# Kernel optimization log

Hardware: AMD Instinct MI355X
Metric: run time of the kernel (lower is better)

Reference implementation:

```python
import jax, jax.numpy as jnp
import numpy as np
from jax import lax

D_STATE = 16
D_CONV = 4
EXPAND = 2


def setup_inputs() -> dict:
    key = jax.random.key(0)
    ks = jax.random.split(key, 12)
    B, C, H, W = 8, 192, 32, 32
    d_inner = EXPAND * C            # 384
    dt_rank = (C + 15) // 16        # 12
    s = lambda k, shape, sc=0.02: jax.random.normal(k, shape, jnp.float32) * sc
    return {
        "x": jax.random.normal(ks[0], (B, C, H, W), jnp.float32),
        # proj_in: 1x1 Conv2d (in_ch -> out_ch)
        "proj_w": s(ks[1], (C, C)),
        "proj_b": s(ks[2], (C,)),
        # Mamba params (mamba_ssm defaults, biases per reference impl)
        "in_proj_w": s(ks[3], (2 * d_inner, C)),
        "conv_w": s(ks[4], (d_inner, D_CONV)),
        "conv_b": s(ks[5], (d_inner,)),
        "xproj_w": s(ks[6], (dt_rank + 2 * D_STATE, d_inner)),
        "dtproj_w": s(ks[7], (d_inner, dt_rank), 0.1),
        "dtproj_b": s(ks[8], (d_inner,), 0.5),
        "A_log": jnp.log(jnp.tile(jnp.arange(1, D_STATE + 1, dtype=jnp.float32), (d_inner, 1))),
        "Dp": jnp.ones((d_inner,), jnp.float32),
        "out_w": s(ks[9], (C, d_inner)),
    }


def _forward(x, proj_w, proj_b, in_proj_w, conv_w, conv_b, xproj_w,
             dtproj_w, dtproj_b, A_log, Dp, out_w):
    B, C, H, W = x.shape
    L = H * W
    # proj_in (1x1 conv) + flatten 'b c h w -> b (h w) c'
    u = jnp.einsum('bchw,oc->bhwo', x, proj_w).reshape(B, L, -1) + proj_b
    # Mamba layer
    xz = u @ in_proj_w.T                      # [B,L,2*d_inner]
    xin, z = jnp.split(xz, 2, axis=-1)
    # causal depthwise conv1d (kernel D_CONV), truncated to L
    xp = jnp.pad(xin, ((0, 0), (D_CONV - 1, 0), (0, 0)))
    xc = conv_b + sum(conv_w[:, k] * xp[:, k:k + L, :] for k in range(D_CONV))
    xc = jax.nn.silu(xc)
    # input-dependent dt, B, C
    dt_rank = dtproj_w.shape[1]
    x_dbl = xc @ xproj_w.T                    # [B,L,dt_rank+2*n]
    dtr, Bt, Ct = jnp.split(x_dbl, [dt_rank, dt_rank + D_STATE], axis=-1)
    dt = jax.nn.softplus(dtr @ dtproj_w.T + dtproj_b)   # [B,L,d_inner]
    A = -jnp.exp(A_log)                       # [d_inner, n]
    deltaA = jnp.exp(dt[..., None] * A)                          # [B,L,d,n]
    dBx = dt[..., None] * Bt[:, :, None, :] * xc[..., None]      # [B,L,d,n]

    def step(h, ins):
        dA, dbx, ct = ins                      # [B,d,n],[B,d,n],[B,n]
        h = dA * h + dbx
        return h, jnp.einsum('bdn,bn->bd', h, ct)

    h0 = jnp.zeros((B, A.shape[0], D_STATE), xc.dtype)
    _, ys = lax.scan(step, h0, (deltaA.transpose(1, 0, 2, 3),
                                dBx.transpose(1, 0, 2, 3),
                                Ct.transpose(1, 0, 2)))
    y = ys.transpose(1, 0, 2) + xc * Dp        # [B,L,d_inner]
    y = y * jax.nn.silu(z)
    out = y @ out_w.T                          # [B,L,C]
    # 'b (h w) c -> b c h w'
    return out.reshape(B, H, W, C).transpose(0, 3, 1, 2)


def reference(x, proj_w, proj_b, in_proj_w, conv_w, conv_b, xproj_w,
              dtproj_w, dtproj_b, A_log, Dp, out_w):
    return _forward(x, proj_w, proj_b, in_proj_w, conv_w, conv_b, xproj_w,
                    dtproj_w, dtproj_b, A_log, Dp, out_w)
```

## Files before the change

kernel.cpp:

```cpp
#include <hip/hip_runtime.h>
#include <math.h>

#define BB 8
#define CC 192
#define LL 1024
#define RT 8192
#define DI 384
#define DT_RANK 12
#define NS 16
#define NSEG 16
#define SEGL 64

typedef __attribute__((ext_vector_type(8))) short bf16x8;
typedef __attribute__((ext_vector_type(4))) float f32x4;

__device__ __forceinline__ unsigned short f2bf(float f) {
    unsigned u = __float_as_uint(f);
    unsigned r = (u + 0x7FFFu + ((u >> 16) & 1u)) >> 16;
    return (unsigned short)r;
}
__device__ __forceinline__ float bf2f(unsigned short h) {
    return __uint_as_float(((unsigned)h) << 16);
}

#define DPPF(v, ctrl) __int_as_float(__builtin_amdgcn_update_dpp(0, __float_as_int(v), ctrl, 0xF, 0xF, true))

__global__ void fuse_w_kernel(const float* __restrict__ in_proj_w,
                              const float* __restrict__ proj_w,
                              const float* __restrict__ proj_b,
                              const float* __restrict__ out_w,
                              unsigned short* __restrict__ W2hi,
                              unsigned short* __restrict__ W2lo,
                              unsigned short* __restrict__ owhi,
                              unsigned short* __restrict__ owlo,
                              float* __restrict__ bias2,
                              float* __restrict__ xdT) {
    int j = blockIdx.x;
    int cp = threadIdx.x;
    int gtid = j * CC + cp;
    for (int i = gtid; i < 44 * RT; i += 768 * CC) xdT[i] = 0.f;
    if (j < DI) {
        float v = out_w[cp * DI + j];
        unsigned short h = f2bf(v);
        owhi[cp * DI + j] = h;
        owlo[cp * DI + j] = f2bf(v - bf2f(h));
    }
    __shared__ float wrow[CC];
    wrow[cp] = in_proj_w[j * CC + cp];
    __syncthreads();
    float acc = 0.f;
#pragma unroll 4
    for (int c = 0; c < CC; ++c) acc = fmaf(wrow[c], proj_w[c * CC + cp], acc);
    unsigned short h = f2bf(acc);
    W2hi[j * CC + cp] = h;
    W2lo[j * CC + cp] = f2bf(acc - bf2f(h));
    if (cp == 0) {
        float b = 0.f;
        for (int c = 0; c < CC; ++c) b = fmaf(wrow[c], proj_b[c], b);
        bias2[j] = b;
    }
}

__global__ __launch_bounds__(256) void gemm_xz(const float* __restrict__ x,
                                               const unsigned short* __restrict__ W2hi,
                                               const unsigned short* __restrict__ W2lo,
                                               const float* __restrict__ bias2,
                                               float* __restrict__ xzT) {
    __shared__ unsigned short xhi[2048];
    __shared__ unsigned short xlo[2048];
    int r0 = blockIdx.x * 64;
    int j0 = blockIdx.y * 128;
    int b  = r0 >> 10;
    int l0 = r0 & 1023;
    int tid = threadIdx.x;
    int lane = tid & 63;
    int wid = tid >> 6;
    int jw = j0 + wid * 16;
    const float* xb = x + b * CC * LL + l0 + lane;
    f32x4 z4 = {0.f, 0.f, 0.f, 0.f};
    f32x4 acc[2][4] = {{z4, z4, z4, z4}, {z4, z4, z4, z4}};
    int arow = lane & 15;
    int akb  = (lane >> 4) * 8;
    for (int ks = 0; ks < 6; ++ks) {
        int k0 = ks * 32;
        float v[8];
#pragma unroll
        for (int e = 0; e < 8; ++e) v[e] = xb[(k0 + wid * 8 + e) * LL];
        union U8 { unsigned short u[8]; bf16x8 v8; } hv, lv;
#pragma unroll
        for (int e = 0; e < 8; ++e) {
            unsigned short h = f2bf(v[e]);
            hv.u[e] = h;
            lv.u[e] = f2bf(v[e] - bf2f(h));
        }
        *(bf16x8*)&xhi[(wid * 64 + lane) * 8] = hv.v8;
        *(bf16x8*)&xlo[(wid * 64 + lane) * 8] = lv.v8;
        __syncthreads();
        int aoff0 = (jw + arow) * CC + k0 + akb;
        int aoff1 = aoff0 + 64 * CC;
        bf16x8 ah0 = *(const bf16x8*)&W2hi[aoff0];
        bf16x8 al0 = *(const bf16x8*)&W2lo[aoff0];
        bf16x8 ah1 = *(const bf16x8*)&W2hi[aoff1];
        bf16x8 al1 = *(const bf16x8*)&W2lo[aoff1];
#pragma unroll
        for (int rt = 0; rt < 4; ++rt) {
            int boff = ((lane >> 4) * 64 + rt * 16 + (lane & 15)) * 8;
            bf16x8 bh = *(const bf16x8*)&xhi[boff];
            bf16x8 bl = *(const bf16x8*)&xlo[boff];
            acc[0][rt] = __builtin_amdgcn_mfma_f32_16x16x32_bf16(ah0, bh, acc[0][rt], 0, 0, 0);
            acc[0][rt] = __builtin_amdgcn_mfma_f32_16x16x32_bf16(ah0, bl, acc[0][rt], 0, 0, 0);
            acc[0][rt] = __builtin_amdgcn_mfma_f32_16x16x32_bf16(al0, bh, acc[0][rt], 0, 0, 0);
            acc[1][rt] = __builtin_amdgcn_mfma_f32_16x16x32_bf16(ah1, bh, acc[1][rt], 0, 0, 0);
            acc[1][rt] = __builtin_amdgcn_mfma_f32_16x16x32_bf16(ah1, bl, acc[1][rt], 0, 0, 0);
            acc[1][rt] = __builtin_amdgcn_mfma_f32_16x16x32_bf16(al1, bh, acc[1][rt], 0, 0, 0);
        }
        __syncthreads();
    }
    bool is_z = (j0 >= DI);
#pragma unroll
    for (int js = 0; js < 2; ++js) {
#pragma unroll
        for (int rt = 0; rt < 4; ++rt) {
            int rbase = r0 + rt * 16 + (lane & 15);
#pragma unroll
            for (int reg = 0; reg < 4; ++reg) {
                int j = jw + js * 64 + (lane >> 4) * 4 + reg;
                float o = acc[js][rt][reg] + bias2[j];
                if (is_z) o = __fdividef(o, 1.f + __expf(-o));
                xzT[j * RT + rbase] = o;
            }
        }
    }
}

__global__ __launch_bounds__(512) void xproj_conv_gemm(const float* __restrict__ xzT,
                                                       const float* __restrict__ conv_w,
                                                       const float* __restrict__ conv_b,
                                                       const float* __restrict__ aw,
                                                       float* __restrict__ xcT,
                                                       float* __restrict__ xdT) {
    __shared__ float Bs[32][64];
    int col0 = blockIdx.x * 64;
    int kbase = blockIdx.y * 96;
    int tid = threadIdx.x;
    int col = tid & 63, mg = tid >> 6;
    int mb = mg * 6;
    const float* ar[6];
#pragma unroll
    for (int m = 0; m < 6; ++m) ar[m] = aw + min(mb + m, 43) * DI + kbase;
    float acc[6] = {};
    int ks = tid >> 4, c4 = (tid & 15) * 4;
    bool atL0 = ((col0 & 1023) == 0) && (c4 == 0);
    for (int k0 = 0; k0 < 96; k0 += 32) {
        int dch = kbase + k0 + ks;
        const float* src = xzT + (size_t)dch * RT + col0 + c4;
        float4 cur = *(const float4*)src;
        float4 prev = make_float4(0.f, 0.f, 0.f, 0.f);
        if (!atL0) prev = *(const float4*)(src - 4);
        float4 w4 = *(const float4*)&conv_w[dch * 4];
        float bb = conv_b[dch];
        float v0 = bb + w4.w * cur.x + w4.z * prev.w + w4.y * prev.z + w4.x * prev.y;
        float v1 = bb + w4.w * cur.y + w4.z * cur.x  + w4.y * prev.w + w4.x * prev.z;
        float v2 = bb + w4.w * cur.z + w4.z * cur.y  + w4.y * cur.x  + w4.x * prev.w;
        float v3 = bb + w4.w * cur.w + w4.z * cur.z  + w4.y * cur.y  + w4.x * cur.x;
        float4 o;
        o.x = __fdividef(v0, 1.f + __expf(-v0));
        o.y = __fdividef(v1, 1.f + __expf(-v1));
        o.z = __fdividef(v2, 1.f + __expf(-v2));
        o.w = __fdividef(v3, 1.f + __expf(-v3));
        *(float4*)&Bs[ks][c4] = o;
        *(float4*)&xcT[(size_t)dch * RT + col0 + c4] = o;
        __syncthreads();
#pragma unroll
        for (int k = 0; k < 32; ++k) {
            float bv = Bs[k][col];
#pragma unroll
            for (int m = 0; m < 6; ++m)
                acc[m] = fmaf(ar[m][k0 + k], bv, acc[m]);
        }
        __syncthreads();
    }
#pragma unroll
    for (int m = 0; m < 6; ++m)
        if (mb + m < 44)
            atomicAdd(&xdT[(mb + m) * RT + col0 + col], acc[m]);
}

__global__ __launch_bounds__(256) void scan_part1(const float* __restrict__ xdT,
                                                  const float* __restrict__ xcT,
                                                  const float* __restrict__ dtw,
                                                  const float* __restrict__ dtb,
                                                  const float* __restrict__ A_log,
                                                  float* __restrict__ P,
                                                  float* __restrict__ Hf) {
    __shared__ float dt_s[16][68], g_s[16][68], B_s[16][68];
    __shared__ float dtr_s[12][68];
    __shared__ float dtw_s[192];
    __shared__ float dtb_s[16];
    int seg = blockIdx.x, d0 = blockIdx.y * 16, b = blockIdx.z;
    int row0 = b * LL + seg * SEGL;
    int tid = threadIdx.x;
    int lane = tid & 63;
    int n = lane & 15;
    int dl = ((tid >> 6) << 2) | (lane >> 4);
    int tdd = tid >> 4, ti = tid & 15;
    if (tid < 192) dtw_s[tid] = dtw[d0 * DT_RANK + tid];
    if (tid < 16)  dtb_s[tid] = dtb[d0 + tid];
    float a = -__expf(A_log[(d0 + dl) * NS + n]);
    *(float4*)&B_s[tdd][ti * 4] = *(const float4*)&xdT[(12 + tdd) * RT + row0 + ti * 4];
    if (tid < 192)
        *(float4*)&dtr_s[tid >> 4][ti * 4] = *(const float4*)&xdT[(tid >> 4) * RT + row0 + ti * 4];
    float4 xv4 = *(const float4*)&xcT[(d0 + tdd) * RT + row0 + ti * 4];
    float xv[4] = {xv4.x, xv4.y, xv4.z, xv4.w};
    __syncthreads();
#pragma unroll
    for (int q = 0; q < 4; ++q) {
        int col = ti * 4 + q;
        float acc = dtb_s[tdd];
#pragma unroll
        for (int rr = 0; rr < DT_RANK; ++rr)
            acc = fmaf(dtr_s[rr][col], dtw_s[tdd * DT_RANK + rr], acc);
        float dtv = fmaxf(acc, 0.f) + __logf(1.f + __expf(-fabsf(acc)));
        dt_s[tdd][col] = dtv;
        g_s[tdd][col]  = dtv * xv[q];
    }
    __syncthreads();
    float h = 0.f, sdt = 0.f;
    for (int ch = 0; ch < 4; ++ch) {
        int c0 = ch * 16;
        float dv[16], gb[16];
#pragma unroll
        for (int q = 0; q < 4; ++q) {
            float4 d4 = *(const float4*)&dt_s[dl][c0 + q * 4];
            float4 g4 = *(const float4*)&g_s[dl][c0 + q * 4];
            float4 b4 = *(const float4*)&B_s[n][c0 + q * 4];
            dv[q * 4 + 0] = d4.x; dv[q * 4 + 1] = d4.y;
            dv[q * 4 + 2] = d4.z; dv[q * 4 + 3] = d4.w;
            gb[q * 4 + 0] = g4.x * b4.x; gb[q * 4 + 1] = g4.y * b4.y;
            gb[q * 4 + 2] = g4.z * b4.z; gb[q * 4 + 3] = g4.w * b4.w;
        }
        float eh[16];
#pragma unroll
        for (int i = 0; i < 16; ++i) eh[i] = __expf(dv[i] * a);
#pragma unroll
        for (int i = 0; i < 16; ++i) {
            sdt += dv[i];
            h = fmaf(eh[i], h, gb[i]);
        }
    }
    int idx = ((seg * BB + b) * DI + d0 + dl) * NS + n;
    P[idx] = __expf(a * sdt);
    Hf[idx] = h;
}

__global__ __launch_bounds__(256) void scan_part2(const float* __restrict__ xdT,
                                                  const float* __restrict__ xcT,
                                                  const float* __restrict__ zsT,
                                                  const float* __restrict__ dtw,
                                                  const float* __restrict__ dtb,
                                                  const float* __restrict__ P,
                                                  const float* __restrict__ Hf,
                                                  const float* __restrict__ A_log,
                                                  const float* __restrict__ Dp,
                                                  float* __restrict__ yT) {
    __shared__ float dt_s[16][68], g_s[16][68], B_s[16][68], C_s[16][68];
    __shared__ float dtr_s[12][68];
    __shared__ float dtw_s[192];
    __shared__ float dtb_s[16];
    int seg = blockIdx.x, d0 = blockIdx.y * 16, b = blockIdx.z;
    int row0 = b * LL + seg * SEGL;
    int tid = threadIdx.x;
    int lane = tid & 63;
    int n = lane & 15;
    int dl = ((tid >> 6) << 2) | (lane >> 4);
    int d = d0 + dl;
    int tdd = tid >> 4, ti = tid & 15;
    if (tid < 192) dtw_s[tid] = dtw[d0 * DT_RANK + tid];
    if (tid < 16)  dtb_s[tid] = dtb[d0 + tid];
    float a = -__expf(A_log[d * NS + n]);
    float Dpd = Dp[d];
    bool b3 = (n & 8) != 0, b2 = (n & 4) != 0, b1 = (n & 2) != 0, b0 = (n & 1) != 0;
    *(float4*)&B_s[tdd][ti * 4] = *(const float4*)&xdT[(12 + tdd) * RT + row0 + ti * 4];
    *(float4*)&C_s[tdd][ti * 4] = *(const float4*)&xdT[(28 + tdd) * RT + row0 + ti * 4];
    if (tid < 192)
        *(float4*)&dtr_s[tid >> 4][ti * 4] = *(const float4*)&xdT[(tid >> 4) * RT + row0 + ti * 4];
    float4 xv4 = *(const float4*)&xcT[(d0 + tdd) * RT + row0 + ti * 4];
    float xv[4] = {xv4.x, xv4.y, xv4.z, xv4.w};
    float h = 0.f;
    for (int s = 0; s < seg; ++s) {
        int off = ((s * BB + b) * DI + d) * NS + n;
        h = fmaf(P[off], h, Hf[off]);
    }
    __syncthreads();
#pragma unroll
    for (int q = 0; q < 4; ++q) {
        int col = ti * 4 + q;
        float acc = dtb_s[tdd];
#pragma unroll
        for (int rr = 0; rr < DT_RANK; ++rr)
            acc = fmaf(dtr_s[rr][col], dtw_s[tdd * DT_RANK + rr], acc);
        float dtv = fmaxf(acc, 0.f) + __logf(1.f + __expf(-fabsf(acc)));
        dt_s[tdd][col] = dtv;
        g_s[tdd][col]  = dtv * xv[q];
    }
    __syncthreads();
    for (int ch = 0; ch < 4; ++ch) {
        int c0 = ch * 16;
        int r = row0 + c0;
        float xr = xcT[(size_t)d * RT + r + n];
        float zr = zsT[(size_t)d * RT + r + n];
        float dv[16], gb[16], cv[16];
#pragma unroll
        for (int q = 0; q < 4; ++q) {
            float4 d4 = *(const float4*)&dt_s[dl][c0 + q * 4];
            float4 g4 = *(const float4*)&g_s[dl][c0 + q * 4];
            float4 b4 = *(const float4*)&B_s[n][c0 + q * 4];
            float4 c4 = *(const float4*)&C_s[n][c0 + q * 4];
            dv[q * 4 + 0] = d4.x; dv[q * 4 + 1] = d4.y;
            dv[q * 4 + 2] = d4.z; dv[q * 4 + 3] = d4.w;
            gb[q * 4 + 0] = g4.x * b4.x; gb[q * 4 + 1] = g4.y * b4.y;
            gb[q * 4 + 2] = g4.z * b4.z; gb[q * 4 + 3] = g4.w * b4.w;
            cv[q * 4 + 0] = c4.x; cv[q * 4 + 1] = c4.y;
            cv[q * 4 + 2] = c4.z; cv[q * 4 + 3] = c4.w;
        }
        float eh[16];
#pragma unroll
        for (int i = 0; i < 16; ++i) eh[i] = __expf(dv[i] * a);
        float w[16];
#pragma unroll
        for (int i = 0; i < 16; ++i) {
            h = fmaf(eh[i], h, gb[i]);
            w[i] = h * cv[i];
        }
        float A8[8];
#pragma unroll
        for (int jj = 0; jj < 8; ++jj) {
            float snd = b3 ? w[jj] : w[jj + 8];
            float rcv = DPPF(snd, 0x140);
            A8[jj] = (b3 ? w[jj + 8] : w[jj]) + rcv;
        }
        float A4[4];
#pragma unroll
        for (int jj = 0; jj < 4; ++jj) {
            float snd = b2 ? A8[jj] : A8[jj + 4];
            float rcv = DPPF(snd, 0x141);
            A4[jj] = (b2 ? A8[jj + 4] : A8[jj]) + rcv;
        }
        float A2[2];
#pragma unroll
        for (int jj = 0; jj < 2; ++jj) {
            float s2 = b1 ? A4[jj] : A4[jj + 2];
            float rcv = DPPF(s2, 0x4E);
            A2[jj] = (b1 ? A4[jj + 2] : A4[jj]) + rcv;
        }
        float s1 = b0 ? A2[0] : A2[1];
        float rcv1 = DPPF(s1, 0xB1);
        float yacc = (b0 ? A2[1] : A2[0]) + rcv1;
        yT[(size_t)d * RT + r + n] = fmaf(xr, Dpd, yacc) * zr;
    }
}

__global__ __launch_bounds__(256) void gemm_out(const float* __restrict__ yT,
                                                const unsigned short* __restrict__ owhi,
                                                const unsigned short* __restrict__ owlo,
                                                float* __restrict__ out) {
    __shared__ unsigned short yhi[2048];
    __shared__ unsigned short ylo[2048];
    int r0 = blockIdx.x * 64;
    int c0 = blockIdx.y * 64;
    int b  = r0 >> 10;
    int l0 = r0 & 1023;
    int tid = threadIdx.x;
    int lane = tid & 63;
    int wid = tid >> 6;
    int cw = c0 + wid * 16;
    const float* yb = yT + r0 + lane;
    f32x4 z4 = {0.f, 0.f, 0.f, 0.f};
    f32x4 acc[4] = {z4, z4, z4, z4};
    int arow = cw + (lane & 15);
    int akb  = (lane >> 4) * 8;
    for (int ks = 0; ks < 12; ++ks) {
        int k0 = ks * 32;
        float v[8];
#pragma unroll
        for (int e = 0; e < 8; ++e) v[e] = yb[(size_t)(k0 + wid * 8 + e) * RT];
        union U8 { unsigned short u[8]; bf16x8 v8; } hv, lv;
#pragma unroll
        for (int e = 0; e < 8; ++e) {
            unsigned short h = f2bf(v[e]);
            hv.u[e] = h;
            lv.u[e] = f2bf(v[e] - bf2f(h));
        }
        *(bf16x8*)&yhi[(wid * 64 + lane) * 8] = hv.v8;
        *(bf16x8*)&ylo[(wid * 64 + lane) * 8] = lv.v8;
        __syncthreads();
        int aoff = arow * DI + k0 + akb;
        bf16x8 ah = *(const bf16x8*)&owhi[aoff];
        bf16x8 al = *(const bf16x8*)&owlo[aoff];
#pragma unroll
        for (int rt = 0; rt < 4; ++rt) {
            int boff = ((lane >> 4) * 64 + rt * 16 + (lane & 15)) * 8;
            bf16x8 bh = *(const bf16x8*)&yhi[boff];
            bf16x8 bl = *(const bf16x8*)&ylo[boff];
            acc[rt] = __builtin_amdgcn_mfma_f32_16x16x32_bf16(ah, bh, acc[rt], 0, 0, 0);
            acc[rt] = __builtin_amdgcn_mfma_f32_16x16x32_bf16(ah, bl, acc[rt], 0, 0, 0);
            acc[rt] = __builtin_amdgcn_mfma_f32_16x16x32_bf16(al, bh, acc[rt], 0, 0, 0);
        }
        __syncthreads();
    }
    float* ob = out + b * CC * LL;
#pragma unroll
    for (int rt = 0; rt < 4; ++rt) {
        int lbase = l0 + rt * 16 + (lane & 15);
#pragma unroll
        for (int reg = 0; reg < 4; ++reg) {
            int c = cw + (lane >> 4) * 4 + reg;
            ob[c * LL + lbase] = acc[rt][reg];
        }
    }
}

extern "C" void kernel_launch(void* const* d_in, const int* in_sizes, int n_in,
                              void* d_out, int out_size, void* d_ws, size_t ws_size,
                              hipStream_t stream) {
    const float* x         = (const float*)d_in[0];
    const float* proj_w    = (const float*)d_in[1];
    const float* proj_b    = (const float*)d_in[2];
    const float* in_proj_w = (const float*)d_in[3];
    const float* conv_w    = (const float*)d_in[4];
    const float* conv_b    = (const float*)d_in[5];
    const float* xproj_w   = (const float*)d_in[6];
    const float* dtproj_w  = (const float*)d_in[7];
    const float* dtproj_b  = (const float*)d_in[8];
    const float* A_log     = (const float*)d_in[9];
    const float* Dp        = (const float*)d_in[10];
    const float* out_w     = (const float*)d_in[11];
    float* out = (float*)d_out;

    float* ws    = (float*)d_ws;
    unsigned short* W2hi = (unsigned short*)ws;
    unsigned short* W2lo = (unsigned short*)(ws + 73728);
    float* bias2 = ws + 147456;
    float* xzT   = bias2 + 768;
    float* xcT   = xzT + 6291456;
    float* yT    = xcT + 3145728;
    float* xdT   = yT + 3145728;
    float* P     = xdT + 360448;
    float* Hf    = P + 786432;
    unsigned short* owhi = (unsigned short*)(Hf + 786432);
    unsigned short* owlo = (unsigned short*)(Hf + 786432 + 36864);
    float* zsT   = xzT + DI * RT;

    fuse_w_kernel<<<768, 192, 0, stream>>>(in_proj_w, proj_w, proj_b, out_w,
                                           W2hi, W2lo, owhi, owlo, bias2, xdT);
    gemm_xz<<<dim3(128, 6), 256, 0, stream>>>(x, W2hi, W2lo, bias2, xzT);
    xproj_conv_gemm<<<dim3(128, 4), 512, 0, stream>>>(xzT, conv_w, conv_b,
                                                      xproj_w, xcT, xdT);
    scan_part1<<<dim3(15, 24, 8), 256, 0, stream>>>(xdT, xcT, dtproj_w, dtproj_b,
                                                    A_log, P, Hf);
    scan_part2<<<dim3(16, 24, 8), 256, 0, stream>>>(xdT, xcT, zsT, dtproj_w, dtproj_b,
                                                    P, Hf, A_log, Dp, yT);
    gemm_out<<<dim3(128, 3), 256, 0, stream>>>(yT, owhi, owlo, out);
}
```

Before: 192.3 us.

## Interleave scan carry buffers, prefetch x/z loads, and double K-step in gemm_out

Scan part 1 now writes the segment decay and final state as one interleaved float2 array, so part 2's cross-segment prefix reads one 8-byte value per step instead of two separate loads. Part 2 also loads its xc and z values for all four chunks up front instead of inside the chunk loop. gemm_out processes 64 K-elements per barrier pair using two LDS buffers, halving the number of sync rounds. The fused-weight kernel reads the shared weight row as float4, a small change in a one-off prep kernel. Costs are more registers and more LDS in gemm_out, which may reduce occupancy.

```diff
diff --git a/kernel.cpp b/kernel.cpp
--- a/kernel.cpp
+++ b/kernel.cpp
@@ -49,8 +49,15 @@
     wrow[cp] = in_proj_w[j * CC + cp];
     __syncthreads();
     float acc = 0.f;
+    const float4* wrow4 = (const float4*)wrow;
 #pragma unroll 4
-    for (int c = 0; c < CC; ++c) acc = fmaf(wrow[c], proj_w[c * CC + cp], acc);
+    for (int c4 = 0; c4 < CC; c4 += 4) {
+        float4 w4 = wrow4[c4 >> 2];
+        acc = fmaf(w4.x, proj_w[(c4 + 0) * CC + cp], acc);
+        acc = fmaf(w4.y, proj_w[(c4 + 1) * CC + cp], acc);
+        acc = fmaf(w4.z, proj_w[(c4 + 2) * CC + cp], acc);
+        acc = fmaf(w4.w, proj_w[(c4 + 3) * CC + cp], acc);
+    }
     unsigned short h = f2bf(acc);
     W2hi[j * CC + cp] = h;
     W2lo[j * CC + cp] = f2bf(acc - bf2f(h));
@@ -191,8 +198,7 @@
                                                   const float* __restrict__ dtw,
                                                   const float* __restrict__ dtb,
                                                   const float* __restrict__ A_log,
-                                                  float* __restrict__ P,
-                                                  float* __restrict__ Hf) {
+                                                  float2* __restrict__ PH) {
     __shared__ float dt_s[16][68], g_s[16][68], B_s[16][68];
     __shared__ float dtr_s[12][68];
     __shared__ float dtw_s[192];
@@ -249,8 +255,7 @@
         }
     }
     int idx = ((seg * BB + b) * DI + d0 + dl) * NS + n;
-    P[idx] = __expf(a * sdt);
-    Hf[idx] = h;
+    PH[idx] = make_float2(__expf(a * sdt), h);
 }
 
 __global__ __launch_bounds__(256) void scan_part2(const float* __restrict__ xdT,
@@ -258,8 +263,7 @@
                                                   const float* __restrict__ zsT,
                                                   const float* __restrict__ dtw,
                                                   const float* __restrict__ dtb,
-                                                  const float* __restrict__ P,
-                                                  const float* __restrict__ Hf,
+                                                  const float2* __restrict__ PH,
                                                   const float* __restrict__ A_log,
                                                   const float* __restrict__ Dp,
                                                   float* __restrict__ yT) {
@@ -286,10 +290,16 @@
         *(float4*)&dtr_s[tid >> 4][ti * 4] = *(const float4*)&xdT[(tid >> 4) * RT + row0 + ti * 4];
     float4 xv4 = *(const float4*)&xcT[(d0 + tdd) * RT + row0 + ti * 4];
     float xv[4] = {xv4.x, xv4.y, xv4.z, xv4.w};
+    float xr[4], zr[4];
+#pragma unroll
+    for (int ch = 0; ch < 4; ++ch) {
+        xr[ch] = xcT[(size_t)d * RT + row0 + ch * 16 + n];
+        zr[ch] = zsT[(size_t)d * RT + row0 + ch * 16 + n];
+    }
     float h = 0.f;
     for (int s = 0; s < seg; ++s) {
-        int off = ((s * BB + b) * DI + d) * NS + n;
-        h = fmaf(P[off], h, Hf[off]);
+        float2 ph = PH[((s * BB + b) * DI + d) * NS + n];
+        h = fmaf(ph.x, h, ph.y);
     }
     __syncthreads();
 #pragma unroll
@@ -307,8 +317,6 @@
     for (int ch = 0; ch < 4; ++ch) {
         int c0 = ch * 16;
         int r = row0 + c0;
-        float xr = xcT[(size_t)d * RT + r + n];
-        float zr = zsT[(size_t)d * RT + r + n];
         float dv[16], gb[16], cv[16];
 #pragma unroll
         for (int q = 0; q < 4; ++q) {
@@ -356,7 +364,7 @@
         float s1 = b0 ? A2[0] : A2[1];
         float rcv1 = DPPF(s1, 0xB1);
         float yacc = (b0 ? A2[1] : A2[0]) + rcv1;
-        yT[(size_t)d * RT + r + n] = fmaf(xr, Dpd, yacc) * zr;
+        yT[(size_t)d * RT + r + n] = fmaf(xr[ch], Dpd, yacc) * zr[ch];
     }
 }
 
@@ -364,8 +372,8 @@
                                                 const unsigned short* __restrict__ owhi,
                                                 const unsigned short* __restrict__ owlo,
                                                 float* __restrict__ out) {
-    __shared__ unsigned short yhi[2048];
-    __shared__ unsigned short ylo[2048];
+    __shared__ unsigned short yhi[2][2048];
+    __shared__ unsigned short ylo[2][2048];
     int r0 = blockIdx.x * 64;
     int c0 = blockIdx.y * 64;
     int b  = r0 >> 10;
@@ -379,32 +387,41 @@
     f32x4 acc[4] = {z4, z4, z4, z4};
     int arow = cw + (lane & 15);
     int akb  = (lane >> 4) * 8;
-    for (int ks = 0; ks < 12; ++ks) {
-        int k0 = ks * 32;
-        float v[8];
-#pragma unroll
-        for (int e = 0; e < 8; ++e) v[e] = yb[(size_t)(k0 + wid * 8 + e) * RT];
+    for (int ks = 0; ks < 6; ++ks) {
+        int k0 = ks * 64;
+        float v[2][8];
+#pragma unroll
+        for (int hh = 0; hh < 2; ++hh)
+#pragma unroll
+            for (int e = 0; e < 8; ++e)
+                v[hh][e] = yb[(size_t)(k0 + hh * 32 + wid * 8 + e) * RT];
         union U8 { unsigned short u[8]; bf16x8 v8; } hv, lv;
 #pragma unroll
-        for (int e = 0; e < 8; ++e) {
-            unsigned short h = f2bf(v[e]);
-            hv.u[e] = h;
-            lv.u[e] = f2bf(v[e] - bf2f(h));
-        }
-        *(bf16x8*)&yhi[(wid * 64 + lane) * 8] = hv.v8;
-        *(bf16x8*)&ylo[(wid * 64 + lane) * 8] = lv.v8;
-        __syncthreads();
-        int aoff = arow * DI + k0 + akb;
-        bf16x8 ah = *(const bf16x8*)&owhi[aoff];
-        bf16x8 al = *(const bf16x8*)&owlo[aoff];
-#pragma unroll
-        for (int rt = 0; rt < 4; ++rt) {
-            int boff = ((lane >> 4) * 64 + rt * 16 + (lane & 15)) * 8;
-            bf16x8 bh = *(const bf16x8*)&yhi[boff];
-            bf16x8 bl = *(const bf16x8*)&ylo[boff];
-            acc[rt] = __builtin_amdgcn_mfma_f32_16x16x32_bf16(ah, bh, acc[rt], 0, 0, 0);
-            acc[rt] = __builtin_amdgcn_mfma_f32_16x16x32_bf16(ah, bl, acc[rt], 0, 0, 0);
-            acc[rt] = __builtin_amdgcn_mfma_f32_16x16x32_bf16(al, bh, acc[rt], 0, 0, 0);
+        for (int hh = 0; hh < 2; ++hh) {
+#pragma unroll
+            for (int e = 0; e < 8; ++e) {
+                unsigned short hb = f2bf(v[hh][e]);
+                hv.u[e] = hb;
+                lv.u[e] = f2bf(v[hh][e] - bf2f(hb));
+            }
+            *(bf16x8*)&yhi[hh][(wid * 64 + lane) * 8] = hv.v8;
+            *(bf16x8*)&ylo[hh][(wid * 64 + lane) * 8] = lv.v8;
+        }
+        __syncthreads();
+#pragma unroll
+        for (int hh = 0; hh < 2; ++hh) {
+            int aoff = arow * DI + k0 + hh * 32 + akb;
+            bf16x8 ah = *(const bf16x8*)&owhi[aoff];
+            bf16x8 al = *(const bf16x8*)&owlo[aoff];
+#pragma unroll
+            for (int rt = 0; rt < 4; ++rt) {
+                int boff = ((lane >> 4) * 64 + rt * 16 + (lane & 15)) * 8;
+                bf16x8 bh = *(const bf16x8*)&yhi[hh][boff];
+                bf16x8 bl = *(const bf16x8*)&ylo[hh][boff];
+                acc[rt] = __builtin_amdgcn_mfma_f32_16x16x32_bf16(ah, bh, acc[rt], 0, 0, 0);
+                acc[rt] = __builtin_amdgcn_mfma_f32_16x16x32_bf16(ah, bl, acc[rt], 0, 0, 0);
+                acc[rt] = __builtin_amdgcn_mfma_f32_16x16x32_bf16(al, bh, acc[rt], 0, 0, 0);
+            }
         }
         __syncthreads();
     }
@@ -445,10 +462,9 @@
     float* xcT   = xzT + 6291456;
     float* yT    = xcT + 3145728;
     float* xdT   = yT + 3145728;
-    float* P     = xdT + 360448;
-    float* Hf    = P + 786432;
-    unsigned short* owhi = (unsigned short*)(Hf + 786432);
-    unsigned short* owlo = (unsigned short*)(Hf + 786432 + 36864);
+    float2* PH   = (float2*)(xdT + 360448);
+    unsigned short* owhi = (unsigned short*)(xdT + 360448 + 1572864);
+    unsigned short* owlo = (unsigned short*)(xdT + 360448 + 1572864 + 36864);
     float* zsT   = xzT + DI * RT;
 
     fuse_w_kernel<<<768, 192, 0, stream>>>(in_proj_w, proj_w, proj_b, out_w,
@@ -457,8 +473,8 @@
     xproj_conv_gemm<<<dim3(128, 4), 512, 0, stream>>>(xzT, conv_w, conv_b,
                                                       xproj_w, xcT, xdT);
     scan_part1<<<dim3(15, 24, 8), 256, 0, stream>>>(xdT, xcT, dtproj_w, dtproj_b,
-                                                    A_log, P, Hf);
+                                                    A_log, PH);
     scan_part2<<<dim3(16, 24, 8), 256, 0, stream>>>(xdT, xcT, zsT, dtproj_w, dtproj_b,
-                                                    P, Hf, A_log, Dp, yT);
+                                                    PH, A_log, Dp, yT);
     gemm_out<<<dim3(128, 3), 256, 0, stream>>>(yT, owhi, owlo, out);
 }
```

New measurement: 182.9 us. 1.05x faster.
